# Optimization experiments

Hardware: AMD Instinct MI355X
Metric: run time of the kernel (lower is better)

## Reference

```python
import jax, jax.numpy as jnp
import numpy as np

B, D, H, O, E = 1048576, 17, 8, 6, 4  # batch, input_dim, expert_hidden, output_dim, n_clusters
G1, G2 = 64, 32  # gating hidden dims


def setup_inputs() -> dict:
    key = jax.random.key(0)
    ks = jax.random.split(key, 14)
    def w(k, shape, fan_in):
        return (jax.random.normal(k, shape, jnp.float32) / jnp.sqrt(jnp.float32(fan_in)))
    return {
        "x": jax.random.normal(ks[0], (B, D), jnp.float32),
        # per-expert MLP params, stacked on leading expert axis E
        "eW1": w(ks[1], (E, D, H), D), "eb1": w(ks[2], (E, H), D),
        "eW2": w(ks[3], (E, H, H), H), "eb2": w(ks[4], (E, H), H),
        "eW3": w(ks[5], (E, H, O), H), "eb3": w(ks[6], (E, O), H),
        # gating classifier params
        "gW1": w(ks[7], (D, G1), D), "gb1": w(ks[8], (G1,), D),
        "gW2": w(ks[9], (G1, G2), G1), "gb2": w(ks[10], (G2,), G1),
        "gW3": w(ks[11], (G2, E), G2), "gb3": w(ks[12], (E,), G2),
    }


def reference(x, eW1, eb1, eW2, eb2, eW3, eb3, gW1, gb1, gW2, gb2, gW3, gb3):
    # gating network: 17 -> 64 -> 32 -> 4 logits
    h = jax.nn.relu(x @ gW1 + gb1)
    h = jax.nn.relu(h @ gW2 + gb2)
    gating_logits = h @ gW3 + gb3  # [B, E]
    selected = jnp.argmax(gating_logits, axis=1)  # [B] hard routing
    # all experts computed (as in the original), stacked over expert axis
    e = jax.nn.relu(jnp.einsum('bi,eih->beh', x, eW1) + eb1)   # [B, E, H]
    e = jax.nn.relu(jnp.einsum('beh,ehk->bek', e, eW2) + eb2)  # [B, E, H]
    eo = jnp.einsum('bek,eko->beo', e, eW3) + eb3              # [B, E, O]
    # gather the selected expert's output per sample
    predictions = jnp.take_along_axis(eo, selected[:, None, None], axis=1)[:, 0, :]  # [B, O]
    return predictions, gating_logits
```

## Files before the change

### kernel.cpp

```cpp
#include <hip/hip_runtime.h>

#define BTOT 1048576
#define D 17
#define H 8
#define OUT 6
#define E 4
#define G1 64
#define G2 32
#define CHUNKS 4
#define XSTR 17
#define GTHR 5.0e-3f

typedef float f32x4 __attribute__((ext_vector_type(4)));
typedef float f32x2 __attribute__((ext_vector_type(2)));
typedef short s16x8 __attribute__((ext_vector_type(8)));
typedef unsigned int uint;

union U4S8 { uint u[4]; s16x8 s; };

__device__ __forceinline__ uint bfr(uint u) {
    return (u + 0x7fffu + ((u >> 16) & 1u)) & 0xffff0000u;
}

__device__ __forceinline__ void wsplit2(float a, float b, uint &hp, uint &lp) {
    uint ha = bfr(__float_as_uint(a));
    uint hb = bfr(__float_as_uint(b));
    float ra = a - __uint_as_float(ha);
    float rb = b - __uint_as_float(hb);
    hp = (ha >> 16) | (hb & 0xffff0000u);
    lp = (bfr(__float_as_uint(ra)) >> 16) | (bfr(__float_as_uint(rb)) & 0xffff0000u);
}

__device__ __forceinline__ void split8t(const float* p, s16x8 &fh, s16x8 &fm, s16x8 &fl) {
    U4S8 Hh, Mm, Ll;
    #pragma unroll
    for (int i = 0; i < 4; ++i) {
        float a = p[2 * i], b = p[2 * i + 1];
        uint ua = __float_as_uint(a), ub = __float_as_uint(b);
        Hh.u[i] = __builtin_amdgcn_perm(ub, ua, 0x07060302u);
        float ra = a - __uint_as_float(ua & 0xffff0000u);
        float rb = b - __uint_as_float(ub & 0xffff0000u);
        uint ura = __float_as_uint(ra), urb = __float_as_uint(rb);
        Mm.u[i] = __builtin_amdgcn_perm(urb, ura, 0x07060302u);
        float sa = ra - __uint_as_float(ura & 0xffff0000u);
        float sb = rb - __uint_as_float(urb & 0xffff0000u);
        Ll.u[i] = __builtin_amdgcn_perm(__float_as_uint(sb), __float_as_uint(sa), 0x07060302u);
    }
    fh = Hh.s; fm = Mm.s; fl = Ll.s;
}

#define MM5(dacc, ah, am, al, bh, bl)                                            \
    dacc = __builtin_amdgcn_mfma_f32_16x16x32_bf16(am, bl, dacc, 0, 0, 0);       \
    dacc = __builtin_amdgcn_mfma_f32_16x16x32_bf16(al, bh, dacc, 0, 0, 0);       \
    dacc = __builtin_amdgcn_mfma_f32_16x16x32_bf16(ah, bl, dacc, 0, 0, 0);       \
    dacc = __builtin_amdgcn_mfma_f32_16x16x32_bf16(am, bh, dacc, 0, 0, 0);       \
    dacc = __builtin_amdgcn_mfma_f32_16x16x32_bf16(ah, bh, dacc, 0, 0, 0);

#define WSTR 292

__global__ __launch_bounds__(256, 2) void hybrid_ruc_kernel(
    const float* __restrict__ x,
    const float* __restrict__ eW1, const float* __restrict__ eb1,
    const float* __restrict__ eW2, const float* __restrict__ eb2,
    const float* __restrict__ eW3, const float* __restrict__ eb3,
    const float* __restrict__ gW1, const float* __restrict__ gb1,
    const float* __restrict__ gW2, const float* __restrict__ gb2,
    const float* __restrict__ gW3, const float* __restrict__ gb3,
    float* __restrict__ out)
{
    __shared__ __align__(16) float sscr[4][1024];
    __shared__ __align__(16) float swl[E * WSTR];
    __shared__ __align__(16) float sxp[256 * XSTR + 16];

    const int tid = threadIdx.x;
    const int wv  = tid >> 6;
    const int ln  = tid & 63;
    const int g   = ln >> 4;
    const int nn  = ln & 15;
    float* scr = sscr[wv];

    if (tid < 16) sxp[256 * XSTR + tid] = 0.0f;
    for (int t = tid; t < E * D * H; t += 256) {
        swl[(t / 136) * WSTR + (t % 136)] = eW1[t];
    }
    if (tid < E * H * H) {
        swl[(tid / 64) * WSTR + 144 + (tid % 64)] = eW2[tid];
    }
    if (tid < E * H * OUT) {
        int e = tid / 48, r = tid % 48, k = r / 6, o = r % 6;
        swl[e * WSTR + 216 + k * 8 + o] = eW3[tid];
    }
    if (tid < E * H) swl[(tid / 8) * WSTR + 136 + (tid % 8)] = eb1[tid];
    if (tid < E * H) swl[(tid / 8) * WSTR + 208 + (tid % 8)] = eb2[tid];
    if (tid < E * OUT) swl[(tid / 6) * WSTR + 280 + (tid % 6)] = eb3[tid];

    {
        const float* gs = x + (long long)blockIdx.x * (CHUNKS * 256 * D) + wv * (64 * D);
        float* ls = &sxp[wv * (64 * D)];
        #pragma unroll
        for (int i = 0; i < D; ++i) ls[i * 64 + ln] = gs[i * 64 + ln];
    }

    float cb1[4], cb2[2], cb3;
    #pragma unroll
    for (int ct = 0; ct < 4; ++ct) cb1[ct] = gb1[ct * 16 + nn];
    cb2[0] = gb2[nn]; cb2[1] = gb2[16 + nn];
    cb3 = (nn < 4) ? gb3[nn] : 0.0f;

    s16x8 B1h[4], B1l[4];
    #pragma unroll
    for (int ct = 0; ct < 4; ++ct) {
        U4S8 Hh, Ll;
        #pragma unroll
        for (int j2 = 0; j2 < 4; ++j2) {
            const int k0 = g * 8 + 2 * j2, n = ct * 16 + nn;
            const float a = (k0 < D)     ? gW1[k0 * G1 + n]       : 0.0f;
            const float b = (k0 + 1 < D) ? gW1[(k0 + 1) * G1 + n] : 0.0f;
            wsplit2(a, b, Hh.u[j2], Ll.u[j2]);
        }
        B1h[ct] = Hh.s; B1l[ct] = Ll.s;
    }
    s16x8 B2h[2][2], B2l[2][2];
    #pragma unroll
    for (int ct = 0; ct < 2; ++ct)
        #pragma unroll
        for (int kt = 0; kt < 2; ++kt) {
            U4S8 Hh, Ll;
            #pragma unroll
            for (int j2 = 0; j2 < 4; ++j2) {
                const int k0 = kt * 32 + g * 8 + 2 * j2, n = ct * 16 + nn;
                wsplit2(gW2[k0 * G2 + n], gW2[(k0 + 1) * G2 + n], Hh.u[j2], Ll.u[j2]);
            }
            B2h[ct][kt] = Hh.s; B2l[ct][kt] = Ll.s;
        }
    s16x8 B3h, B3l;
    {
        U4S8 Hh, Ll;
        #pragma unroll
        for (int j2 = 0; j2 < 4; ++j2) {
            const int k0 = g * 8 + 2 * j2;
            const float a = (nn < 4) ? gW3[k0 * E + nn]       : 0.0f;
            const float b = (nn < 4) ? gW3[(k0 + 1) * E + nn] : 0.0f;
            wsplit2(a, b, Hh.u[j2], Ll.u[j2]);
        }
        B3h = Hh.s; B3l = Ll.s;
    }

    __syncthreads();

    #pragma unroll 1
    for (int c = 0; c < CHUNKS; ++c) {
        const long long cbase = ((long long)blockIdx.x * CHUNKS + c) * 256;
        if (c) {
            const float* gs = x + cbase * D + wv * (64 * D);
            float* ls = &sxp[wv * (64 * D)];
            #pragma unroll
            for (int i = 0; i < D; ++i) ls[i * 64 + ln] = gs[i * 64 + ln];
        }

        f32x4 Lg[4];
        #pragma unroll
        for (int rt = 0; rt < 4; ++rt) {
            const int srow = wv * 64 + rt * 16 + nn;
            float xv[8];
            const int xb = srow * XSTR + ((g == 3) ? 0 : g * 8);
            #pragma unroll
            for (int j = 0; j < 8; ++j) xv[j] = sxp[xb + j];
            s16x8 a1h, a1m, a1l; split8t(xv, a1h, a1m, a1l);

            #pragma unroll
            for (int ct = 0; ct < 4; ++ct) {
                f32x4 d = {cb1[ct], cb1[ct], cb1[ct], cb1[ct]};
                MM5(d, a1h, a1m, a1l, B1h[ct], B1l[ct]);
                #pragma unroll
                for (int r = 0; r < 4; ++r) {
                    float hv = fmaxf(d[r], 0.0f);
                    int s = g * 4 + r, n = ct * 16 + nn;
                    scr[s * 64 + (((n >> 2) ^ (s & 15)) << 2) + (n & 3)] = hv;
                }
            }

            s16x8 a2h[2], a2m[2], a2l[2];
            #pragma unroll
            for (int kt = 0; kt < 2; ++kt) {
                int kb0 = kt * 8 + g * 2;
                float hv8[8];
                *(f32x4*)&hv8[0] = *(const f32x4*)(&scr[nn * 64 + ((kb0 ^ (nn & 15)) << 2)]);
                *(f32x4*)&hv8[4] = *(const f32x4*)(&scr[nn * 64 + (((kb0 + 1) ^ (nn & 15)) << 2)]);
                split8t(hv8, a2h[kt], a2m[kt], a2l[kt]);
            }

            #pragma unroll
            for (int ct = 0; ct < 2; ++ct) {
                f32x4 d = {cb2[ct], cb2[ct], cb2[ct], cb2[ct]};
                #pragma unroll
                for (int kt = 0; kt < 2; ++kt) {
                    MM5(d, a2h[kt], a2m[kt], a2l[kt], B2h[ct][kt], B2l[ct][kt]);
                }
                #pragma unroll
                for (int r = 0; r < 4; ++r) {
                    float hv = fmaxf(d[r], 0.0f);
                    int s = g * 4 + r, n = ct * 16 + nn;
                    scr[s * 32 + (((n >> 2) ^ (s & 7)) << 2) + (n & 3)] = hv;
                }
            }

            float h28[8];
            *(f32x4*)&h28[0] = *(const f32x4*)(&scr[nn * 32 + (((2 * g) ^ (nn & 7)) << 2)]);
            *(f32x4*)&h28[4] = *(const f32x4*)(&scr[nn * 32 + (((2 * g + 1) ^ (nn & 7)) << 2)]);
            s16x8 a3h, a3m, a3l; split8t(h28, a3h, a3m, a3l);

            f32x4 d3 = {cb3, cb3, cb3, cb3};
            MM5(d3, a3h, a3m, a3l, B3h, B3l);
            Lg[rt] = d3;
        }

        if (nn < 4) {
            #pragma unroll
            for (int rt = 0; rt < 4; ++rt)
                #pragma unroll
                for (int r = 0; r < 4; ++r)
                    scr[(rt * 16 + g * 4 + r) * 4 + nn] = Lg[rt][r];
        }
        f32x4 lgv = *(const f32x4*)(&scr[ln * 4]);

        int sel = 0;
        {
            float b = lgv.x;
            if (lgv.y > b) { b = lgv.y; sel = 1; }
            if (lgv.z > b) { b = lgv.z; sel = 2; }
            if (lgv.w > b) { b = lgv.w; sel = 3; }
        }
        float mx01 = fmaxf(lgv.x, lgv.y), mn01 = fminf(lgv.x, lgv.y);
        float mx23 = fmaxf(lgv.z, lgv.w), mn23 = fminf(lgv.z, lgv.w);
        float best   = fmaxf(mx01, mx23);
        float second = fmaxf(fminf(mx01, mx23), (mx01 >= mx23) ? mn01 : mn23);

        unsigned long long fmask = __ballot(best - second < GTHR);
        if (fmask) {
            do {
                int sl = (int)__builtin_ctzll(fmask);
                fmask &= (fmask - 1);
                const int fr = wv * 64 + sl;
                float h1j = gb1[ln];
                #pragma unroll 1
                for (int i = 0; i < D; ++i)
                    h1j = __builtin_fmaf(sxp[fr * XSTR + i], gW1[i * G1 + ln], h1j);
                scr[ln] = fmaxf(h1j, 0.0f);
                int j2 = ln & 31;
                float h2j = gb2[j2];
                #pragma unroll 4
                for (int c2 = 0; c2 < G1; ++c2)
                    h2j = __builtin_fmaf(scr[c2], gW2[c2 * G2 + j2], h2j);
                scr[64 + j2] = fmaxf(h2j, 0.0f);
                int e = ln & 3;
                float lge = gb3[e];
                #pragma unroll 4
                for (int jj = 0; jj < G2; ++jj)
                    lge = __builtin_fmaf(scr[64 + jj], gW3[jj * E + e], lge);
                float l0 = __shfl(lge, 0), l1 = __shfl(lge, 1);
                float l2 = __shfl(lge, 2), l3 = __shfl(lge, 3);
                int s2 = 0; float bb = l0;
                if (l1 > bb) { bb = l1; s2 = 1; }
                if (l2 > bb) { bb = l2; s2 = 2; }
                if (l3 > bb) { bb = l3; s2 = 3; }
                if (ln == sl) sel = s2;
            } while (fmask);
        }

        const float* xrow = &sxp[tid * XSTR];
        const float* wl = &swl[sel * WSTR];

        float t1[H];
        {
            f32x4 ba = *(const f32x4*)(wl + 136);
            f32x4 bb = *(const f32x4*)(wl + 140);
            t1[0]=ba.x; t1[1]=ba.y; t1[2]=ba.z; t1[3]=ba.w;
            t1[4]=bb.x; t1[5]=bb.y; t1[6]=bb.z; t1[7]=bb.w;
        }
        #pragma unroll
        for (int i = 0; i < D; ++i) {
            const float xi = xrow[i];
            f32x4 wa = *(const f32x4*)(wl + i * 8);
            f32x4 wb = *(const f32x4*)(wl + i * 8 + 4);
            t1[0] = __builtin_fmaf(xi, wa.x, t1[0]);
            t1[1] = __builtin_fmaf(xi, wa.y, t1[1]);
            t1[2] = __builtin_fmaf(xi, wa.z, t1[2]);
            t1[3] = __builtin_fmaf(xi, wa.w, t1[3]);
            t1[4] = __builtin_fmaf(xi, wb.x, t1[4]);
            t1[5] = __builtin_fmaf(xi, wb.y, t1[5]);
            t1[6] = __builtin_fmaf(xi, wb.z, t1[6]);
            t1[7] = __builtin_fmaf(xi, wb.w, t1[7]);
        }
        float t2[H];
        {
            f32x4 ba = *(const f32x4*)(wl + 208);
            f32x4 bb = *(const f32x4*)(wl + 212);
            t2[0]=ba.x; t2[1]=ba.y; t2[2]=ba.z; t2[3]=ba.w;
            t2[4]=bb.x; t2[5]=bb.y; t2[6]=bb.z; t2[7]=bb.w;
        }
        #pragma unroll
        for (int k = 0; k < H; ++k) {
            const float tv = fmaxf(t1[k], 0.0f);
            f32x4 wa = *(const f32x4*)(wl + 144 + k * 8);
            f32x4 wb = *(const f32x4*)(wl + 144 + k * 8 + 4);
            t2[0] = __builtin_fmaf(tv, wa.x, t2[0]);
            t2[1] = __builtin_fmaf(tv, wa.y, t2[1]);
            t2[2] = __builtin_fmaf(tv, wa.z, t2[2]);
            t2[3] = __builtin_fmaf(tv, wa.w, t2[3]);
            t2[4] = __builtin_fmaf(tv, wb.x, t2[4]);
            t2[5] = __builtin_fmaf(tv, wb.y, t2[5]);
            t2[6] = __builtin_fmaf(tv, wb.z, t2[6]);
            t2[7] = __builtin_fmaf(tv, wb.w, t2[7]);
        }
        float pred[OUT];
        {
            f32x4 ba = *(const f32x4*)(wl + 280);
            pred[0]=ba.x; pred[1]=ba.y; pred[2]=ba.z; pred[3]=ba.w;
            pred[4]=wl[284]; pred[5]=wl[285];
        }
        #pragma unroll
        for (int k = 0; k < H; ++k) {
            const float tv = fmaxf(t2[k], 0.0f);
            f32x4 wa = *(const f32x4*)(wl + 216 + k * 8);
            f32x2 wb = *(const f32x2*)(wl + 216 + k * 8 + 4);
            pred[0] = __builtin_fmaf(tv, wa.x, pred[0]);
            pred[1] = __builtin_fmaf(tv, wa.y, pred[1]);
            pred[2] = __builtin_fmaf(tv, wa.z, pred[2]);
            pred[3] = __builtin_fmaf(tv, wa.w, pred[3]);
            pred[4] = __builtin_fmaf(tv, wb.x, pred[4]);
            pred[5] = __builtin_fmaf(tv, wb.y, pred[5]);
        }

        const long long b = cbase + tid;
        f32x2 p0 = {pred[0], pred[1]};
        f32x2 p1 = {pred[2], pred[3]};
        f32x2 p2 = {pred[4], pred[5]};
        *(f32x2*)(out + b * 6)     = p0;
        *(f32x2*)(out + b * 6 + 2) = p1;
        *(f32x2*)(out + b * 6 + 4) = p2;
        float* lout = out + (long long)BTOT * OUT;
        *(f32x4*)(lout + b * 4) = lgv;
    }
}

extern "C" void kernel_launch(void* const* d_in, const int* in_sizes, int n_in,
                              void* d_out, int out_size, void* d_ws, size_t ws_size,
                              hipStream_t stream) {
    const float* x   = (const float*)d_in[0];
    const float* eW1 = (const float*)d_in[1];
    const float* eb1 = (const float*)d_in[2];
    const float* eW2 = (const float*)d_in[3];
    const float* eb2 = (const float*)d_in[4];
    const float* eW3 = (const float*)d_in[5];
    const float* eb3 = (const float*)d_in[6];
    const float* gW1 = (const float*)d_in[7];
    const float* gb1 = (const float*)d_in[8];
    const float* gW2 = (const float*)d_in[9];
    const float* gb2 = (const float*)d_in[10];
    const float* gW3 = (const float*)d_in[11];
    const float* gb3 = (const float*)d_in[12];
    float* out = (float*)d_out;

    dim3 grid(BTOT / (256 * CHUNKS)), block(256);
    hipLaunchKernelGGL(hybrid_ruc_kernel, grid, block, 0, stream,
                       x, eW1, eb1, eW2, eb2, eW3, eb3,
                       gW1, gb1, gW2, gb2, gW3, gb3, out);
}
```

Baseline: 240.7 us.

## Use single-pass fp16 MFMA for gating and drop chunk loop

Replaces the 5-pass bf16 split MFMA gating network with one fp16 MFMA per tile, converting activations with packed round-to-zero conversion and weights with a direct fp16 cast. It raises the fallback threshold for ambiguous rows that are recomputed in fp32. It also removes the per-block chunk loop, so each block handles 256 rows with a 4x larger grid, and x is loaded with a flat coalesced copy. The goal is to cut MFMA count and split arithmetic. The cost is lower gating precision, which depends on the wider fp32 fallback to keep the argmax correct, plus more per-block weight setup overhead.

```diff
diff --git a/kernel.cpp b/kernel.cpp
--- a/kernel.cpp
+++ b/kernel.cpp
@@ -7,56 +7,19 @@
 #define E 4
 #define G1 64
 #define G2 32
-#define CHUNKS 4
-#define XSTR 17
-#define GTHR 5.0e-3f
+#define GTHR 1.0e-2f
 
 typedef float f32x4 __attribute__((ext_vector_type(4)));
 typedef float f32x2 __attribute__((ext_vector_type(2)));
-typedef short s16x8 __attribute__((ext_vector_type(8)));
-typedef unsigned int uint;
-
-union U4S8 { uint u[4]; s16x8 s; };
-
-__device__ __forceinline__ uint bfr(uint u) {
-    return (u + 0x7fffu + ((u >> 16) & 1u)) & 0xffff0000u;
-}
-
-__device__ __forceinline__ void wsplit2(float a, float b, uint &hp, uint &lp) {
-    uint ha = bfr(__float_as_uint(a));
-    uint hb = bfr(__float_as_uint(b));
-    float ra = a - __uint_as_float(ha);
-    float rb = b - __uint_as_float(hb);
-    hp = (ha >> 16) | (hb & 0xffff0000u);
-    lp = (bfr(__float_as_uint(ra)) >> 16) | (bfr(__float_as_uint(rb)) & 0xffff0000u);
-}
-
-__device__ __forceinline__ void split8t(const float* p, s16x8 &fh, s16x8 &fm, s16x8 &fl) {
-    U4S8 Hh, Mm, Ll;
-    #pragma unroll
-    for (int i = 0; i < 4; ++i) {
-        float a = p[2 * i], b = p[2 * i + 1];
-        uint ua = __float_as_uint(a), ub = __float_as_uint(b);
-        Hh.u[i] = __builtin_amdgcn_perm(ub, ua, 0x07060302u);
-        float ra = a - __uint_as_float(ua & 0xffff0000u);
-        float rb = b - __uint_as_float(ub & 0xffff0000u);
-        uint ura = __float_as_uint(ra), urb = __float_as_uint(rb);
-        Mm.u[i] = __builtin_amdgcn_perm(urb, ura, 0x07060302u);
-        float sa = ra - __uint_as_float(ura & 0xffff0000u);
-        float sb = rb - __uint_as_float(urb & 0xffff0000u);
-        Ll.u[i] = __builtin_amdgcn_perm(__float_as_uint(sb), __float_as_uint(sa), 0x07060302u);
-    }
-    fh = Hh.s; fm = Mm.s; fl = Ll.s;
-}
-
-#define MM5(dacc, ah, am, al, bh, bl)                                            \
-    dacc = __builtin_amdgcn_mfma_f32_16x16x32_bf16(am, bl, dacc, 0, 0, 0);       \
-    dacc = __builtin_amdgcn_mfma_f32_16x16x32_bf16(al, bh, dacc, 0, 0, 0);       \
-    dacc = __builtin_amdgcn_mfma_f32_16x16x32_bf16(ah, bl, dacc, 0, 0, 0);       \
-    dacc = __builtin_amdgcn_mfma_f32_16x16x32_bf16(am, bh, dacc, 0, 0, 0);       \
-    dacc = __builtin_amdgcn_mfma_f32_16x16x32_bf16(ah, bh, dacc, 0, 0, 0);
-
-#define WSTR 292
+typedef __fp16 h16x2 __attribute__((ext_vector_type(2)));
+typedef __fp16 h16x8 __attribute__((ext_vector_type(8)));
+
+union UH8 { h16x2 p[4]; h16x8 v; };
+
+#define MMF(dacc, a, b) \
+    dacc = __builtin_amdgcn_mfma_f32_16x16x32_f16(a, b, dacc, 0, 0, 0);
+
+#define WSTR 296
 
 __global__ __launch_bounds__(256, 2) void hybrid_ruc_kernel(
     const float* __restrict__ x,
@@ -68,18 +31,25 @@
     const float* __restrict__ gW3, const float* __restrict__ gb3,
     float* __restrict__ out)
 {
+    __shared__ float sx[256 * D + 16];
+    __shared__ __align__(16) float swl[E * WSTR];
     __shared__ __align__(16) float sscr[4][1024];
-    __shared__ __align__(16) float swl[E * WSTR];
-    __shared__ __align__(16) float sxp[256 * XSTR + 16];
 
     const int tid = threadIdx.x;
     const int wv  = tid >> 6;
     const int ln  = tid & 63;
     const int g   = ln >> 4;
     const int nn  = ln & 15;
+    const long long bbase = (long long)blockIdx.x * 256;
     float* scr = sscr[wv];
 
-    if (tid < 16) sxp[256 * XSTR + tid] = 0.0f;
+    #pragma unroll
+    for (int k = 0; k < D; ++k) {
+        int t = tid + k * 256;
+        sx[t] = x[bbase * D + t];
+    }
+    if (tid < 16) sx[256 * D + tid] = 0.0f;
+
     for (int t = tid; t < E * D * H; t += 256) {
         swl[(t / 136) * WSTR + (t % 136)] = eW1[t];
     }
@@ -94,254 +64,240 @@
     if (tid < E * H) swl[(tid / 8) * WSTR + 208 + (tid % 8)] = eb2[tid];
     if (tid < E * OUT) swl[(tid / 6) * WSTR + 280 + (tid % 6)] = eb3[tid];
 
-    {
-        const float* gs = x + (long long)blockIdx.x * (CHUNKS * 256 * D) + wv * (64 * D);
-        float* ls = &sxp[wv * (64 * D)];
-        #pragma unroll
-        for (int i = 0; i < D; ++i) ls[i * 64 + ln] = gs[i * 64 + ln];
-    }
-
     float cb1[4], cb2[2], cb3;
     #pragma unroll
     for (int ct = 0; ct < 4; ++ct) cb1[ct] = gb1[ct * 16 + nn];
     cb2[0] = gb2[nn]; cb2[1] = gb2[16 + nn];
     cb3 = (nn < 4) ? gb3[nn] : 0.0f;
 
-    s16x8 B1h[4], B1l[4];
+    h16x8 B1f[4];
     #pragma unroll
     for (int ct = 0; ct < 4; ++ct) {
-        U4S8 Hh, Ll;
-        #pragma unroll
-        for (int j2 = 0; j2 < 4; ++j2) {
-            const int k0 = g * 8 + 2 * j2, n = ct * 16 + nn;
-            const float a = (k0 < D)     ? gW1[k0 * G1 + n]       : 0.0f;
-            const float b = (k0 + 1 < D) ? gW1[(k0 + 1) * G1 + n] : 0.0f;
-            wsplit2(a, b, Hh.u[j2], Ll.u[j2]);
-        }
-        B1h[ct] = Hh.s; B1l[ct] = Ll.s;
-    }
-    s16x8 B2h[2][2], B2l[2][2];
+        UH8 u;
+        #pragma unroll
+        for (int j = 0; j < 8; ++j) {
+            const int k = g * 8 + j, n = ct * 16 + nn;
+            u.v[j] = (__fp16)((k < D) ? gW1[k * G1 + n] : 0.0f);
+        }
+        B1f[ct] = u.v;
+    }
+    h16x8 B2f[2][2];
     #pragma unroll
     for (int ct = 0; ct < 2; ++ct)
         #pragma unroll
         for (int kt = 0; kt < 2; ++kt) {
-            U4S8 Hh, Ll;
-            #pragma unroll
-            for (int j2 = 0; j2 < 4; ++j2) {
-                const int k0 = kt * 32 + g * 8 + 2 * j2, n = ct * 16 + nn;
-                wsplit2(gW2[k0 * G2 + n], gW2[(k0 + 1) * G2 + n], Hh.u[j2], Ll.u[j2]);
+            UH8 u;
+            #pragma unroll
+            for (int j = 0; j < 8; ++j) {
+                const int k = kt * 32 + g * 8 + j, n = ct * 16 + nn;
+                u.v[j] = (__fp16)gW2[k * G2 + n];
             }
-            B2h[ct][kt] = Hh.s; B2l[ct][kt] = Ll.s;
-        }
-    s16x8 B3h, B3l;
-    {
-        U4S8 Hh, Ll;
-        #pragma unroll
-        for (int j2 = 0; j2 < 4; ++j2) {
-            const int k0 = g * 8 + 2 * j2;
-            const float a = (nn < 4) ? gW3[k0 * E + nn]       : 0.0f;
-            const float b = (nn < 4) ? gW3[(k0 + 1) * E + nn] : 0.0f;
-            wsplit2(a, b, Hh.u[j2], Ll.u[j2]);
-        }
-        B3h = Hh.s; B3l = Ll.s;
-    }
-
+            B2f[ct][kt] = u.v;
+        }
+    h16x8 B3f;
+    {
+        UH8 u;
+        #pragma unroll
+        for (int j = 0; j < 8; ++j) {
+            const int k = g * 8 + j;
+            u.v[j] = (__fp16)((nn < 4) ? gW3[k * E + nn] : 0.0f);
+        }
+        B3f = u.v;
+    }
     __syncthreads();
 
-    #pragma unroll 1
-    for (int c = 0; c < CHUNKS; ++c) {
-        const long long cbase = ((long long)blockIdx.x * CHUNKS + c) * 256;
-        if (c) {
-            const float* gs = x + cbase * D + wv * (64 * D);
-            float* ls = &sxp[wv * (64 * D)];
-            #pragma unroll
-            for (int i = 0; i < D; ++i) ls[i * 64 + ln] = gs[i * 64 + ln];
-        }
-
-        f32x4 Lg[4];
-        #pragma unroll
-        for (int rt = 0; rt < 4; ++rt) {
-            const int srow = wv * 64 + rt * 16 + nn;
-            float xv[8];
-            const int xb = srow * XSTR + ((g == 3) ? 0 : g * 8);
-            #pragma unroll
-            for (int j = 0; j < 8; ++j) xv[j] = sxp[xb + j];
-            s16x8 a1h, a1m, a1l; split8t(xv, a1h, a1m, a1l);
-
-            #pragma unroll
-            for (int ct = 0; ct < 4; ++ct) {
-                f32x4 d = {cb1[ct], cb1[ct], cb1[ct], cb1[ct]};
-                MM5(d, a1h, a1m, a1l, B1h[ct], B1l[ct]);
-                #pragma unroll
-                for (int r = 0; r < 4; ++r) {
-                    float hv = fmaxf(d[r], 0.0f);
-                    int s = g * 4 + r, n = ct * 16 + nn;
-                    scr[s * 64 + (((n >> 2) ^ (s & 15)) << 2) + (n & 3)] = hv;
-                }
+    f32x4 Lg[4];
+    #pragma unroll
+    for (int rt = 0; rt < 4; ++rt) {
+        const int srow = wv * 64 + rt * 16 + nn;
+        UH8 a1;
+        {
+            const int xb = srow * D + ((g == 3) ? 0 : g * 8);
+            #pragma unroll
+            for (int j2 = 0; j2 < 4; ++j2)
+                a1.p[j2] = __builtin_amdgcn_cvt_pkrtz(sx[xb + 2 * j2], sx[xb + 2 * j2 + 1]);
+        }
+
+        #pragma unroll
+        for (int ct = 0; ct < 4; ++ct) {
+            f32x4 d = {cb1[ct], cb1[ct], cb1[ct], cb1[ct]};
+            MMF(d, a1.v, B1f[ct]);
+            #pragma unroll
+            for (int r = 0; r < 4; ++r) {
+                float hv = fmaxf(d[r], 0.0f);
+                int s = g * 4 + r, n = ct * 16 + nn;
+                scr[s * 64 + (((n >> 2) ^ (s & 15)) << 2) + (n & 3)] = hv;
             }
-
-            s16x8 a2h[2], a2m[2], a2l[2];
-            #pragma unroll
-            for (int kt = 0; kt < 2; ++kt) {
-                int kb0 = kt * 8 + g * 2;
-                float hv8[8];
-                *(f32x4*)&hv8[0] = *(const f32x4*)(&scr[nn * 64 + ((kb0 ^ (nn & 15)) << 2)]);
-                *(f32x4*)&hv8[4] = *(const f32x4*)(&scr[nn * 64 + (((kb0 + 1) ^ (nn & 15)) << 2)]);
-                split8t(hv8, a2h[kt], a2m[kt], a2l[kt]);
+        }
+
+        UH8 a2[2];
+        #pragma unroll
+        for (int kt = 0; kt < 2; ++kt) {
+            int kb0 = kt * 8 + g * 2;
+            f32x4 va = *(const f32x4*)(&scr[nn * 64 + ((kb0 ^ nn) << 2)]);
+            f32x4 vb = *(const f32x4*)(&scr[nn * 64 + (((kb0 + 1) ^ nn) << 2)]);
+            a2[kt].p[0] = __builtin_amdgcn_cvt_pkrtz(va.x, va.y);
+            a2[kt].p[1] = __builtin_amdgcn_cvt_pkrtz(va.z, va.w);
+            a2[kt].p[2] = __builtin_amdgcn_cvt_pkrtz(vb.x, vb.y);
+            a2[kt].p[3] = __builtin_amdgcn_cvt_pkrtz(vb.z, vb.w);
+        }
+
+        #pragma unroll
+        for (int ct = 0; ct < 2; ++ct) {
+            f32x4 d = {cb2[ct], cb2[ct], cb2[ct], cb2[ct]};
+            MMF(d, a2[0].v, B2f[ct][0]);
+            MMF(d, a2[1].v, B2f[ct][1]);
+            #pragma unroll
+            for (int r = 0; r < 4; ++r) {
+                float hv = fmaxf(d[r], 0.0f);
+                int s = g * 4 + r, n = ct * 16 + nn;
+                scr[s * 32 + (((n >> 2) ^ (s & 7)) << 2) + (n & 3)] = hv;
             }
-
-            #pragma unroll
-            for (int ct = 0; ct < 2; ++ct) {
-                f32x4 d = {cb2[ct], cb2[ct], cb2[ct], cb2[ct]};
-                #pragma unroll
-                for (int kt = 0; kt < 2; ++kt) {
-                    MM5(d, a2h[kt], a2m[kt], a2l[kt], B2h[ct][kt], B2l[ct][kt]);
-                }
-                #pragma unroll
-                for (int r = 0; r < 4; ++r) {
-                    float hv = fmaxf(d[r], 0.0f);
-                    int s = g * 4 + r, n = ct * 16 + nn;
-                    scr[s * 32 + (((n >> 2) ^ (s & 7)) << 2) + (n & 3)] = hv;
-                }
-            }
-
-            float h28[8];
-            *(f32x4*)&h28[0] = *(const f32x4*)(&scr[nn * 32 + (((2 * g) ^ (nn & 7)) << 2)]);
-            *(f32x4*)&h28[4] = *(const f32x4*)(&scr[nn * 32 + (((2 * g + 1) ^ (nn & 7)) << 2)]);
-            s16x8 a3h, a3m, a3l; split8t(h28, a3h, a3m, a3l);
-
-            f32x4 d3 = {cb3, cb3, cb3, cb3};
-            MM5(d3, a3h, a3m, a3l, B3h, B3l);
-            Lg[rt] = d3;
-        }
-
-        if (nn < 4) {
-            #pragma unroll
-            for (int rt = 0; rt < 4; ++rt)
-                #pragma unroll
-                for (int r = 0; r < 4; ++r)
-                    scr[(rt * 16 + g * 4 + r) * 4 + nn] = Lg[rt][r];
-        }
-        f32x4 lgv = *(const f32x4*)(&scr[ln * 4]);
-
-        int sel = 0;
+        }
+
+        UH8 a3;
         {
-            float b = lgv.x;
-            if (lgv.y > b) { b = lgv.y; sel = 1; }
-            if (lgv.z > b) { b = lgv.z; sel = 2; }
-            if (lgv.w > b) { b = lgv.w; sel = 3; }
-        }
-        float mx01 = fmaxf(lgv.x, lgv.y), mn01 = fminf(lgv.x, lgv.y);
-        float mx23 = fmaxf(lgv.z, lgv.w), mn23 = fminf(lgv.z, lgv.w);
-        float best   = fmaxf(mx01, mx23);
-        float second = fmaxf(fminf(mx01, mx23), (mx01 >= mx23) ? mn01 : mn23);
-
-        unsigned long long fmask = __ballot(best - second < GTHR);
-        if (fmask) {
-            do {
-                int sl = (int)__builtin_ctzll(fmask);
-                fmask &= (fmask - 1);
-                const int fr = wv * 64 + sl;
-                float h1j = gb1[ln];
-                #pragma unroll 1
-                for (int i = 0; i < D; ++i)
-                    h1j = __builtin_fmaf(sxp[fr * XSTR + i], gW1[i * G1 + ln], h1j);
-                scr[ln] = fmaxf(h1j, 0.0f);
-                int j2 = ln & 31;
-                float h2j = gb2[j2];
-                #pragma unroll 4
-                for (int c2 = 0; c2 < G1; ++c2)
-                    h2j = __builtin_fmaf(scr[c2], gW2[c2 * G2 + j2], h2j);
-                scr[64 + j2] = fmaxf(h2j, 0.0f);
-                int e = ln & 3;
-                float lge = gb3[e];
-                #pragma unroll 4
-                for (int jj = 0; jj < G2; ++jj)
-                    lge = __builtin_fmaf(scr[64 + jj], gW3[jj * E + e], lge);
-                float l0 = __shfl(lge, 0), l1 = __shfl(lge, 1);
-                float l2 = __shfl(lge, 2), l3 = __shfl(lge, 3);
-                int s2 = 0; float bb = l0;
-                if (l1 > bb) { bb = l1; s2 = 1; }
-                if (l2 > bb) { bb = l2; s2 = 2; }
-                if (l3 > bb) { bb = l3; s2 = 3; }
-                if (ln == sl) sel = s2;
-            } while (fmask);
-        }
-
-        const float* xrow = &sxp[tid * XSTR];
-        const float* wl = &swl[sel * WSTR];
-
-        float t1[H];
-        {
-            f32x4 ba = *(const f32x4*)(wl + 136);
-            f32x4 bb = *(const f32x4*)(wl + 140);
-            t1[0]=ba.x; t1[1]=ba.y; t1[2]=ba.z; t1[3]=ba.w;
-            t1[4]=bb.x; t1[5]=bb.y; t1[6]=bb.z; t1[7]=bb.w;
-        }
-        #pragma unroll
-        for (int i = 0; i < D; ++i) {
-            const float xi = xrow[i];
-            f32x4 wa = *(const f32x4*)(wl + i * 8);
-            f32x4 wb = *(const f32x4*)(wl + i * 8 + 4);
-            t1[0] = __builtin_fmaf(xi, wa.x, t1[0]);
-            t1[1] = __builtin_fmaf(xi, wa.y, t1[1]);
-            t1[2] = __builtin_fmaf(xi, wa.z, t1[2]);
-            t1[3] = __builtin_fmaf(xi, wa.w, t1[3]);
-            t1[4] = __builtin_fmaf(xi, wb.x, t1[4]);
-            t1[5] = __builtin_fmaf(xi, wb.y, t1[5]);
-            t1[6] = __builtin_fmaf(xi, wb.z, t1[6]);
-            t1[7] = __builtin_fmaf(xi, wb.w, t1[7]);
-        }
-        float t2[H];
-        {
-            f32x4 ba = *(const f32x4*)(wl + 208);
-            f32x4 bb = *(const f32x4*)(wl + 212);
-            t2[0]=ba.x; t2[1]=ba.y; t2[2]=ba.z; t2[3]=ba.w;
-            t2[4]=bb.x; t2[5]=bb.y; t2[6]=bb.z; t2[7]=bb.w;
-        }
-        #pragma unroll
-        for (int k = 0; k < H; ++k) {
-            const float tv = fmaxf(t1[k], 0.0f);
-            f32x4 wa = *(const f32x4*)(wl + 144 + k * 8);
-            f32x4 wb = *(const f32x4*)(wl + 144 + k * 8 + 4);
-            t2[0] = __builtin_fmaf(tv, wa.x, t2[0]);
-            t2[1] = __builtin_fmaf(tv, wa.y, t2[1]);
-            t2[2] = __builtin_fmaf(tv, wa.z, t2[2]);
-            t2[3] = __builtin_fmaf(tv, wa.w, t2[3]);
-            t2[4] = __builtin_fmaf(tv, wb.x, t2[4]);
-            t2[5] = __builtin_fmaf(tv, wb.y, t2[5]);
-            t2[6] = __builtin_fmaf(tv, wb.z, t2[6]);
-            t2[7] = __builtin_fmaf(tv, wb.w, t2[7]);
-        }
-        float pred[OUT];
-        {
-            f32x4 ba = *(const f32x4*)(wl + 280);
-            pred[0]=ba.x; pred[1]=ba.y; pred[2]=ba.z; pred[3]=ba.w;
-            pred[4]=wl[284]; pred[5]=wl[285];
-        }
-        #pragma unroll
-        for (int k = 0; k < H; ++k) {
-            const float tv = fmaxf(t2[k], 0.0f);
-            f32x4 wa = *(const f32x4*)(wl + 216 + k * 8);
-            f32x2 wb = *(const f32x2*)(wl + 216 + k * 8 + 4);
-            pred[0] = __builtin_fmaf(tv, wa.x, pred[0]);
-            pred[1] = __builtin_fmaf(tv, wa.y, pred[1]);
-            pred[2] = __builtin_fmaf(tv, wa.z, pred[2]);
-            pred[3] = __builtin_fmaf(tv, wa.w, pred[3]);
-            pred[4] = __builtin_fmaf(tv, wb.x, pred[4]);
-            pred[5] = __builtin_fmaf(tv, wb.y, pred[5]);
-        }
-
-        const long long b = cbase + tid;
-        f32x2 p0 = {pred[0], pred[1]};
-        f32x2 p1 = {pred[2], pred[3]};
-        f32x2 p2 = {pred[4], pred[5]};
-        *(f32x2*)(out + b * 6)     = p0;
-        *(f32x2*)(out + b * 6 + 2) = p1;
-        *(f32x2*)(out + b * 6 + 4) = p2;
-        float* lout = out + (long long)BTOT * OUT;
-        *(f32x4*)(lout + b * 4) = lgv;
-    }
+            f32x4 va = *(const f32x4*)(&scr[nn * 32 + (((2 * g) ^ (nn & 7)) << 2)]);
+            f32x4 vb = *(const f32x4*)(&scr[nn * 32 + (((2 * g + 1) ^ (nn & 7)) << 2)]);
+            a3.p[0] = __builtin_amdgcn_cvt_pkrtz(va.x, va.y);
+            a3.p[1] = __builtin_amdgcn_cvt_pkrtz(va.z, va.w);
+            a3.p[2] = __builtin_amdgcn_cvt_pkrtz(vb.x, vb.y);
+            a3.p[3] = __builtin_amdgcn_cvt_pkrtz(vb.z, vb.w);
+        }
+
+        f32x4 d3 = {cb3, cb3, cb3, cb3};
+        MMF(d3, a3.v, B3f);
+        Lg[rt] = d3;
+    }
+
+    if (nn < 4) {
+        #pragma unroll
+        for (int rt = 0; rt < 4; ++rt)
+            #pragma unroll
+            for (int r = 0; r < 4; ++r)
+                scr[(rt * 16 + g * 4 + r) * 4 + nn] = Lg[rt][r];
+    }
+    f32x4 lgv = *(const f32x4*)(&scr[ln * 4]);
+
+    int sel = 0;
+    {
+        float b = lgv.x;
+        if (lgv.y > b) { b = lgv.y; sel = 1; }
+        if (lgv.z > b) { b = lgv.z; sel = 2; }
+        if (lgv.w > b) { b = lgv.w; sel = 3; }
+    }
+    float mx01 = fmaxf(lgv.x, lgv.y), mn01 = fminf(lgv.x, lgv.y);
+    float mx23 = fmaxf(lgv.z, lgv.w), mn23 = fminf(lgv.z, lgv.w);
+    float best   = fmaxf(mx01, mx23);
+    float second = fmaxf(fminf(mx01, mx23), (mx01 >= mx23) ? mn01 : mn23);
+
+    unsigned long long fmask = __ballot(best - second < GTHR);
+    if (fmask) {
+        do {
+            int sl = (int)__builtin_ctzll(fmask);
+            fmask &= (fmask - 1);
+            const int fr = wv * 64 + sl;
+            float h1j = gb1[ln];
+            #pragma unroll 1
+            for (int i = 0; i < D; ++i)
+                h1j = __builtin_fmaf(sx[fr * D + i], gW1[i * G1 + ln], h1j);
+            scr[ln] = fmaxf(h1j, 0.0f);
+            int j2 = ln & 31;
+            float h2j = gb2[j2];
+            #pragma unroll 4
+            for (int c2 = 0; c2 < G1; ++c2)
+                h2j = __builtin_fmaf(scr[c2], gW2[c2 * G2 + j2], h2j);
+            scr[64 + j2] = fmaxf(h2j, 0.0f);
+            int e = ln & 3;
+            float lge = gb3[e];
+            #pragma unroll 4
+            for (int jj = 0; jj < G2; ++jj)
+                lge = __builtin_fmaf(scr[64 + jj], gW3[jj * E + e], lge);
+            float l0 = __shfl(lge, 0), l1 = __shfl(lge, 1);
+            float l2 = __shfl(lge, 2), l3 = __shfl(lge, 3);
+            int s2 = 0; float bb = l0;
+            if (l1 > bb) { bb = l1; s2 = 1; }
+            if (l2 > bb) { bb = l2; s2 = 2; }
+            if (l3 > bb) { bb = l3; s2 = 3; }
+            if (ln == sl) sel = s2;
+        } while (fmask);
+    }
+
+    float xr[D];
+    #pragma unroll
+    for (int i = 0; i < D; ++i) xr[i] = sx[tid * D + i];
+    const float* wl = &swl[sel * WSTR];
+
+    float t1[H];
+    {
+        f32x4 ba = *(const f32x4*)(wl + 136);
+        f32x4 bb = *(const f32x4*)(wl + 140);
+        t1[0]=ba.x; t1[1]=ba.y; t1[2]=ba.z; t1[3]=ba.w;
+        t1[4]=bb.x; t1[5]=bb.y; t1[6]=bb.z; t1[7]=bb.w;
+    }
+    #pragma unroll
+    for (int i = 0; i < D; ++i) {
+        const float xi = xr[i];
+        f32x4 wa = *(const f32x4*)(wl + i * 8);
+        f32x4 wb = *(const f32x4*)(wl + i * 8 + 4);
+        t1[0] = __builtin_fmaf(xi, wa.x, t1[0]);
+        t1[1] = __builtin_fmaf(xi, wa.y, t1[1]);
+        t1[2] = __builtin_fmaf(xi, wa.z, t1[2]);
+        t1[3] = __builtin_fmaf(xi, wa.w, t1[3]);
+        t1[4] = __builtin_fmaf(xi, wb.x, t1[4]);
+        t1[5] = __builtin_fmaf(xi, wb.y, t1[5]);
+        t1[6] = __builtin_fmaf(xi, wb.z, t1[6]);
+        t1[7] = __builtin_fmaf(xi, wb.w, t1[7]);
+    }
+    float t2[H];
+    {
+        f32x4 ba = *(const f32x4*)(wl + 208);
+        f32x4 bb = *(const f32x4*)(wl + 212);
+        t2[0]=ba.x; t2[1]=ba.y; t2[2]=ba.z; t2[3]=ba.w;
+        t2[4]=bb.x; t2[5]=bb.y; t2[6]=bb.z; t2[7]=bb.w;
+    }
+    #pragma unroll
+    for (int k = 0; k < H; ++k) {
+        const float tv = fmaxf(t1[k], 0.0f);
+        f32x4 wa = *(const f32x4*)(wl + 144 + k * 8);
+        f32x4 wb = *(const f32x4*)(wl + 144 + k * 8 + 4);
+        t2[0] = __builtin_fmaf(tv, wa.x, t2[0]);
+        t2[1] = __builtin_fmaf(tv, wa.y, t2[1]);
+        t2[2] = __builtin_fmaf(tv, wa.z, t2[2]);
+        t2[3] = __builtin_fmaf(tv, wa.w, t2[3]);
+        t2[4] = __builtin_fmaf(tv, wb.x, t2[4]);
+        t2[5] = __builtin_fmaf(tv, wb.y, t2[5]);
+        t2[6] = __builtin_fmaf(tv, wb.z, t2[6]);
+        t2[7] = __builtin_fmaf(tv, wb.w, t2[7]);
+    }
+    float pred[OUT];
+    {
+        f32x4 ba = *(const f32x4*)(wl + 280);
+        pred[0]=ba.x; pred[1]=ba.y; pred[2]=ba.z; pred[3]=ba.w;
+        pred[4]=wl[284]; pred[5]=wl[285];
+    }
+    #pragma unroll
+    for (int k = 0; k < H; ++k) {
+        const float tv = fmaxf(t2[k], 0.0f);
+        f32x4 wa = *(const f32x4*)(wl + 216 + k * 8);
+        f32x2 wb = *(const f32x2*)(wl + 216 + k * 8 + 4);
+        pred[0] = __builtin_fmaf(tv, wa.x, pred[0]);
+        pred[1] = __builtin_fmaf(tv, wa.y, pred[1]);
+        pred[2] = __builtin_fmaf(tv, wa.z, pred[2]);
+        pred[3] = __builtin_fmaf(tv, wa.w, pred[3]);
+        pred[4] = __builtin_fmaf(tv, wb.x, pred[4]);
+        pred[5] = __builtin_fmaf(tv, wb.y, pred[5]);
+    }
+
+    const long long b = bbase + tid;
+    f32x2 p0 = {pred[0], pred[1]};
+    f32x2 p1 = {pred[2], pred[3]};
+    f32x2 p2 = {pred[4], pred[5]};
+    *(f32x2*)(out + b * 6)     = p0;
+    *(f32x2*)(out + b * 6 + 2) = p1;
+    *(f32x2*)(out + b * 6 + 4) = p2;
+    float* lout = out + (long long)BTOT * OUT;
+    *(f32x4*)(lout + b * 4) = lgv;
 }
 
 extern "C" void kernel_launch(void* const* d_in, const int* in_sizes, int n_in,
@@ -362,7 +318,7 @@
     const float* gb3 = (const float*)d_in[12];
     float* out = (float*)d_out;
 
-    dim3 grid(BTOT / (256 * CHUNKS)), block(256);
+    dim3 grid(BTOT / 256), block(256);
     hipLaunchKernelGGL(hybrid_ruc_kernel, grid, block, 0, stream,
                        x, eW1, eb1, eW2, eb2, eW3, eb3,
                        gW1, gb1, gW2, gb2, gW3, gb3, out);
```

Measured after the change: 241.4 us. No clear change (+0.3%).
